# Performance work log

Measured on AMD Instinct MI355X. Metric: run time of the kernel, lower is better.

The kernel has to match this reference:

```python
import jax, jax.numpy as jnp
import numpy as np

D = 2048  # input_size
H = 2048  # hidden_size
K = 4096  # number of children


def setup_inputs() -> dict:
    key = jax.random.key(0)
    ks = jax.random.split(key, 12)
    sD = 1.0 / np.sqrt(D)
    sH = 1.0 / np.sqrt(H)
    return {
        "input": jax.random.normal(ks[0], (D,), dtype=jnp.float32),
        "children_c": jax.random.normal(ks[1], (K, H), dtype=jnp.float32),
        "children_h": jax.random.normal(ks[2], (K, H), dtype=jnp.float32),
        "W_iou_x": jax.random.uniform(ks[3], (3 * H, D), jnp.float32, -sD, sD),
        "b_iou_x": jax.random.uniform(ks[4], (3 * H,), jnp.float32, -sD, sD),
        "W_iou_h": jax.random.uniform(ks[5], (3 * H, H), jnp.float32, -sH, sH),
        "b_iou_h": jax.random.uniform(ks[6], (3 * H,), jnp.float32, -sH, sH),
        "W_fx": jax.random.uniform(ks[7], (H, D), jnp.float32, -sD, sD),
        "b_fx": jax.random.uniform(ks[8], (H,), jnp.float32, -sD, sD),
        "W_fh": jax.random.uniform(ks[9], (H, H), jnp.float32, -sH, sH),
        "b_fh": jax.random.uniform(ks[10], (H,), jnp.float32, -sH, sH),
    }


def reference(input, children_c, children_h,
              W_iou_x, b_iou_x, W_iou_h, b_iou_h,
              W_fx, b_fx, W_fh, b_fh):
    # iou = iou_x(input) + iou_h(sum_k h_k)  -> [3H]
    h_sum = jnp.sum(children_h, axis=0)
    iou = (W_iou_x @ input + b_iou_x) + (W_iou_h @ h_sum + b_iou_h)
    i, o, u = jnp.split(iou, 3)
    i = jax.nn.sigmoid(i)
    o = jax.nn.sigmoid(o)
    u = jnp.tanh(u)
    # per-child forget gates, batched over K (original loops in Python):
    # f_k = sigmoid(f_x(input) + f_h(h_k))  -> [K, H]
    fx = W_fx @ input + b_fx                       # [H], computed once
    fh = children_h @ W_fh.T + b_fh                # [K, H] GEMM
    f = jax.nn.sigmoid(fx[None, :] + fh)           # [K, H]
    c = i * u + jnp.sum(f * children_c, axis=0)    # [H]
    h = o * jnp.tanh(c)                            # [H]
    return (o, c, h)
```

## Files before the change

### kernel.cpp

```cpp
#include <hip/hip_runtime.h>

typedef unsigned short u16;
typedef short bf16x8 __attribute__((ext_vector_type(8)));
typedef float f32x4 __attribute__((ext_vector_type(4)));

#define D_IN 2048
#define H_DIM 2048
#define K_CH 4096

__device__ __forceinline__ u16 f2bf(float f) {
  unsigned int u = __float_as_uint(f);
  u += 0x7fffu + ((u >> 16) & 1u);
  return (u16)(u >> 16);
}
__device__ __forceinline__ float sigmoidf(float x) {
  return 1.0f / (1.0f + __expf(-x));
}
__device__ __forceinline__ uint4 packrow(float4 a, float4 b) {
  uint4 w;
  w.x = (unsigned)f2bf(a.x) | ((unsigned)f2bf(a.y) << 16);
  w.y = (unsigned)f2bf(a.z) | ((unsigned)f2bf(a.w) << 16);
  w.z = (unsigned)f2bf(b.x) | ((unsigned)f2bf(b.y) << 16);
  w.w = (unsigned)f2bf(b.z) | ((unsigned)f2bf(b.w) << 16);
  return w;
}

__global__ __launch_bounds__(256) void k1(
    const float* __restrict__ ch, const float* __restrict__ wfh,
    const float* __restrict__ Wfx, const float* __restrict__ bfx,
    const float* __restrict__ bfh, const float* __restrict__ x,
    const float* __restrict__ Wix, const float* __restrict__ bix,
    const float* __restrict__ bih, float* __restrict__ partials,
    u16* __restrict__ chb, u16* __restrict__ wfhb, float* __restrict__ g,
    float* __restrict__ ioux, float* __restrict__ hsum,
    float* __restrict__ accv) {
  const int t = threadIdx.x;
  const int bid = blockIdx.x;
  if (bid < 1024) {
    const int r0 = bid * 4;
    float4 a[4], b[4];
#pragma unroll
    for (int r = 0; r < 4; ++r) {
      const float4* p = (const float4*)(ch + (size_t)(r0 + r) * H_DIM + t * 8);
      a[r] = p[0];
      b[r] = p[1];
    }
    float s0 = 0.f, s1 = 0.f, s2 = 0.f, s3 = 0.f;
    float s4 = 0.f, s5 = 0.f, s6 = 0.f, s7 = 0.f;
#pragma unroll
    for (int r = 0; r < 4; ++r) {
      s0 += a[r].x; s1 += a[r].y; s2 += a[r].z; s3 += a[r].w;
      s4 += b[r].x; s5 += b[r].y; s6 += b[r].z; s7 += b[r].w;
      *(uint4*)(chb + (size_t)(r0 + r) * H_DIM + t * 8) = packrow(a[r], b[r]);
    }
    float4 lo, hi;
    lo.x = s0; lo.y = s1; lo.z = s2; lo.w = s3;
    hi.x = s4; hi.y = s5; hi.z = s6; hi.w = s7;
    float* pp = partials + (size_t)bid * H_DIM + t * 8;
    *(float4*)pp = lo;
    *(float4*)(pp + 4) = hi;
  } else if (bid < 1536) {
    const size_t base = (size_t)(bid - 1024) * 8192 + t * 8;
    float4 a[4], b[4];
#pragma unroll
    for (int j = 0; j < 4; ++j) {
      const float4* p = (const float4*)(wfh + base + j * 2048);
      a[j] = p[0];
      b[j] = p[1];
    }
#pragma unroll
    for (int j = 0; j < 4; ++j)
      *(uint4*)(wfhb + base + j * 2048) = packrow(a[j], b[j]);
  } else if (bid < 2048) {
    const int wave = t >> 6, lane = t & 63;
    const int h = (bid - 1536) * 4 + wave;
    const float4* w = (const float4*)(Wfx + (size_t)h * D_IN);
    const float4* xv = (const float4*)x;
    float s = 0.f;
#pragma unroll
    for (int i = 0; i < 8; ++i) {
      int idx = i * 64 + lane;
      float4 av = w[idx], bv = xv[idx];
      s += av.x * bv.x + av.y * bv.y + av.z * bv.z + av.w * bv.w;
    }
#pragma unroll
    for (int off = 32; off > 0; off >>= 1) s += __shfl_xor(s, off);
    if (lane == 0) g[h] = s + bfx[h] + bfh[h];
  } else if (bid < 3584) {
    const int wave = t >> 6, lane = t & 63;
    const int row = (bid - 2048) * 4 + wave;
    const float4* w = (const float4*)(Wix + (size_t)row * D_IN);
    const float4* xv = (const float4*)x;
    float s = 0.f;
#pragma unroll
    for (int i = 0; i < 8; ++i) {
      int idx = i * 64 + lane;
      float4 av = w[idx], bv = xv[idx];
      s += av.x * bv.x + av.y * bv.y + av.z * bv.z + av.w * bv.w;
    }
#pragma unroll
    for (int off = 32; off > 0; off >>= 1) s += __shfl_xor(s, off);
    if (lane == 0) ioux[row] = s + bix[row] + bih[row];
  } else {
    float4 z = {0.f, 0.f, 0.f, 0.f};
    ((float4*)hsum)[t * 2] = z;
    ((float4*)hsum)[t * 2 + 1] = z;
    ((float4*)accv)[t * 2] = z;
    ((float4*)accv)[t * 2 + 1] = z;
  }
}

#define BM 256
#define BN 128
#define BK 64

__global__ __launch_bounds__(512) void kG(
    const u16* __restrict__ chb, const float* __restrict__ cc,
    const u16* __restrict__ wfhb, const float* __restrict__ g,
    const float* __restrict__ partials, float* __restrict__ hsum,
    float* __restrict__ accv) {
  __shared__ u16 As[2][BM * BK];
  __shared__ u16 Bs[2][BN * BK];

  const int bid = blockIdx.x;
  const int t = threadIdx.x;

  if (bid < 64) {
    const int c = (bid & 7) * 256 + (t & 255);
    const int p0 = (bid >> 3) * 128 + (t >> 8) * 64;
    float a0 = 0.f, a1 = 0.f, a2 = 0.f, a3 = 0.f;
    float a4 = 0.f, a5 = 0.f, a6 = 0.f, a7 = 0.f;
    for (int p = p0; p < p0 + 64; p += 8) {
      a0 += partials[(size_t)(p + 0) * H_DIM + c];
      a1 += partials[(size_t)(p + 1) * H_DIM + c];
      a2 += partials[(size_t)(p + 2) * H_DIM + c];
      a3 += partials[(size_t)(p + 3) * H_DIM + c];
      a4 += partials[(size_t)(p + 4) * H_DIM + c];
      a5 += partials[(size_t)(p + 5) * H_DIM + c];
      a6 += partials[(size_t)(p + 6) * H_DIM + c];
      a7 += partials[(size_t)(p + 7) * H_DIM + c];
    }
    float s = ((a0 + a1) + (a2 + a3)) + ((a4 + a5) + (a6 + a7));
    atomicAdd(hsum + c, s);
    return;
  }

  const int gb = bid - 64;
  const int xcd = gb & 7;
  const int u = gb >> 3;
  const int bm = (xcd << 1) | (u >> 4);
  const int bn = u & 15;
  const int row0 = bm * BM;
  const int col0 = bn * BN;

  const int wave = t >> 6, lane = t & 63;
  const int lrow = lane & 15, lquad = lane >> 4;
  const int wm = wave >> 1, wn = wave & 1;

  f32x4 acc[4][4] = {};

  const int srow = lane >> 3;
  const int schunk = (lane & 7) ^ srow;
  const u16* agbase = chb  + (size_t)(row0 + wave * 32 + srow) * H_DIM + schunk * 8;
  const u16* bgbase = wfhb + (size_t)(col0 + wave * 16 + srow) * H_DIM + schunk * 8;

#define STAGE(buf, kb)                                                        \
  do {                                                                        \
    _Pragma("unroll")                                                         \
    for (int i = 0; i < 4; ++i)                                               \
      __builtin_amdgcn_global_load_lds(                                       \
          (const __attribute__((address_space(1))) void*)(agbase + (size_t)i * 8 * H_DIM + (kb) * BK), \
          (__attribute__((address_space(3))) void*)(&As[buf][(wave * 32 + i * 8) * 64]), \
          16, 0, 0);                                                          \
    _Pragma("unroll")                                                         \
    for (int i = 0; i < 2; ++i)                                               \
      __builtin_amdgcn_global_load_lds(                                       \
          (const __attribute__((address_space(1))) void*)(bgbase + (size_t)i * 8 * H_DIM + (kb) * BK), \
          (__attribute__((address_space(3))) void*)(&Bs[buf][(wave * 16 + i * 8) * 64]), \
          16, 0, 0);                                                          \
  } while (0)

#define COMPUTE(buf)                                                          \
  do {                                                                        \
    _Pragma("unroll")                                                         \
    for (int step = 0; step < 2; ++step) {                                    \
      const int slot = ((step * 4 + lquad) ^ (lrow & 7)) * 8;                 \
      bf16x8 fa[4], fb[4];                                                    \
      _Pragma("unroll")                                                       \
      for (int i = 0; i < 4; ++i)                                             \
        fa[i] = *(const bf16x8*)(&As[buf][(wm * 64 + i * 16 + lrow) * 64 + slot]); \
      _Pragma("unroll")                                                       \
      for (int i = 0; i < 4; ++i)                                             \
        fb[i] = *(const bf16x8*)(&Bs[buf][(wn * 64 + i * 16 + lrow) * 64 + slot]); \
      __builtin_amdgcn_s_setprio(1);                                          \
      _Pragma("unroll")                                                       \
      for (int mi = 0; mi < 4; ++mi)                                          \
        _Pragma("unroll")                                                     \
        for (int ni = 0; ni < 4; ++ni)                                        \
          acc[mi][ni] = __builtin_amdgcn_mfma_f32_16x16x32_bf16(              \
              fa[mi], fb[ni], acc[mi][ni], 0, 0, 0);                          \
      __builtin_amdgcn_s_setprio(0);                                          \
    }                                                                         \
  } while (0)

#define VMCNT6() do { asm volatile("s_waitcnt vmcnt(6)" ::: "memory");        \
                      __builtin_amdgcn_sched_barrier(0); } while (0)
#define VMCNT0() do { asm volatile("s_waitcnt vmcnt(0)" ::: "memory");        \
                      __builtin_amdgcn_sched_barrier(0); } while (0)
#define SBAR()   do { __builtin_amdgcn_s_barrier();                           \
                      __builtin_amdgcn_sched_barrier(0); } while (0)

  STAGE(0, 0);
  STAGE(1, 1);

  for (int kb = 0; kb < D_IN / BK - 2; ++kb) {
    const int cur = kb & 1;
    VMCNT6();
    SBAR();
    COMPUTE(cur);
    SBAR();
    STAGE(cur, kb + 2);
  }
  VMCNT6(); SBAR();
  COMPUTE(0);
  SBAR();
  VMCNT0(); SBAR();
  COMPUTE(1);

#pragma unroll
  for (int ni = 0; ni < 4; ++ni) {
    const int colg = col0 + wn * 64 + ni * 16 + lrow;
    const float gv = g[colg];
    float s = 0.f;
#pragma unroll
    for (int mi = 0; mi < 4; ++mi) {
      const int rowg = row0 + wm * 64 + mi * 16 + lquad * 4;
#pragma unroll
      for (int r = 0; r < 4; ++r) {
        float f = sigmoidf(gv + acc[mi][ni][r]);
        s += f * cc[(size_t)(rowg + r) * H_DIM + colg];
      }
    }
    s += __shfl_xor(s, 16);
    s += __shfl_xor(s, 32);
    if (lquad == 0) atomicAdd(accv + colg, s);
  }
#undef STAGE
#undef COMPUTE
#undef VMCNT6
#undef VMCNT0
#undef SBAR
}

__global__ __launch_bounds__(256) void kmvF(const float* __restrict__ Wih,
                                            const float* __restrict__ hsum,
                                            const float* __restrict__ ioux,
                                            const float* __restrict__ accv,
                                            float* __restrict__ out) {
  const int wave = threadIdx.x >> 6, lane = threadIdx.x & 63;
  const int h = blockIdx.x * 4 + wave;
  const float4* w0 = (const float4*)(Wih + (size_t)h * H_DIM);
  const float4* w1 = (const float4*)(Wih + (size_t)(H_DIM + h) * H_DIM);
  const float4* w2 = (const float4*)(Wih + (size_t)(2 * H_DIM + h) * H_DIM);
  const float4* hv = (const float4*)hsum;
  float s0 = 0.f, s1 = 0.f, s2 = 0.f;
#pragma unroll
  for (int i = 0; i < 8; ++i) {
    int idx = i * 64 + lane;
    float4 b = hv[idx];
    float4 a0 = w0[idx], a1 = w1[idx], a2 = w2[idx];
    s0 += a0.x * b.x + a0.y * b.y + a0.z * b.z + a0.w * b.w;
    s1 += a1.x * b.x + a1.y * b.y + a1.z * b.z + a1.w * b.w;
    s2 += a2.x * b.x + a2.y * b.y + a2.z * b.z + a2.w * b.w;
  }
#pragma unroll
  for (int off = 32; off > 0; off >>= 1) {
    s0 += __shfl_xor(s0, off);
    s1 += __shfl_xor(s1, off);
    s2 += __shfl_xor(s2, off);
  }
  if (lane == 0) {
    float i_ = sigmoidf(ioux[h] + s0);
    float o_ = sigmoidf(ioux[H_DIM + h] + s1);
    float u_ = tanhf(ioux[2 * H_DIM + h] + s2);
    float c_ = i_ * u_ + accv[h];
    float hh = o_ * tanhf(c_);
    out[h] = o_;
    out[H_DIM + h] = c_;
    out[2 * H_DIM + h] = hh;
  }
}

extern "C" void kernel_launch(void* const* d_in, const int* in_sizes, int n_in,
                              void* d_out, int out_size, void* d_ws, size_t ws_size,
                              hipStream_t stream) {
  const float* x   = (const float*)d_in[0];
  const float* cc  = (const float*)d_in[1];
  const float* ch  = (const float*)d_in[2];
  const float* Wix = (const float*)d_in[3];
  const float* bix = (const float*)d_in[4];
  const float* Wih = (const float*)d_in[5];
  const float* bih = (const float*)d_in[6];
  const float* Wfx = (const float*)d_in[7];
  const float* bfx = (const float*)d_in[8];
  const float* Wfh = (const float*)d_in[9];
  const float* bfh = (const float*)d_in[10];

  float* ws   = (float*)d_ws;
  float* hsum = ws;
  float* ioux = ws + 2048;
  float* g    = ws + 8192;
  float* accv = ws + 10240;
  float* partials = ws + 12288;
  u16* chb  = (u16*)(ws + 12288 + 1024 * 2048);
  u16* wfhb = chb + (size_t)K_CH * H_DIM;
  float* out = (float*)d_out;

  k1<<<3585, 256, 0, stream>>>(ch, Wfh, Wfx, bfx, bfh, x, Wix, bix, bih,
                               partials, chb, wfhb, g, ioux, hsum, accv);
  kG<<<320, 512, 0, stream>>>(chb, cc, wfhb, g, partials, hsum, accv);
  kmvF<<<512, 256, 0, stream>>>(Wih, hsum, ioux, accv, out);
}
```

Baseline: 258.8 us.

## Triple-buffer LDS and double-buffer register fragments in forget-gate GEMM

Moves the GEMM main loop from two LDS buffers to three with rotating indices. It also double-buffers the MFMA operand fragments in registers, so the LDS reads for the next tile are issued while the MFMAs for the current tile run. The goal is to hide LDS read latency and global-load latency behind matrix-core work. The cost is more LDS per block (lower occupancy possible), double the fragment registers, and more delicate waitcnt accounting that could be wrong.

```diff
diff --git a/kernel.cpp b/kernel.cpp
--- a/kernel.cpp
+++ b/kernel.cpp
@@ -119,8 +119,8 @@
     const u16* __restrict__ wfhb, const float* __restrict__ g,
     const float* __restrict__ partials, float* __restrict__ hsum,
     float* __restrict__ accv) {
-  __shared__ u16 As[2][BM * BK];
-  __shared__ u16 Bs[2][BN * BK];
+  __shared__ u16 As[3][BM * BK];
+  __shared__ u16 Bs[3][BN * BK];
 
   const int bid = blockIdx.x;
   const int t = threadIdx.x;
@@ -158,74 +158,100 @@
   const int wm = wave >> 1, wn = wave & 1;
 
   f32x4 acc[4][4] = {};
+  bf16x8 faA[2][4], fbA[2][4];
+  bf16x8 faB[2][4], fbB[2][4];
 
   const int srow = lane >> 3;
   const int schunk = (lane & 7) ^ srow;
   const u16* agbase = chb  + (size_t)(row0 + wave * 32 + srow) * H_DIM + schunk * 8;
   const u16* bgbase = wfhb + (size_t)(col0 + wave * 16 + srow) * H_DIM + schunk * 8;
 
-#define STAGE(buf, kb)                                                        \
+#define STAGE(bi, kb)                                                         \
   do {                                                                        \
     _Pragma("unroll")                                                         \
     for (int i = 0; i < 4; ++i)                                               \
       __builtin_amdgcn_global_load_lds(                                       \
-          (const __attribute__((address_space(1))) void*)(agbase + (size_t)i * 8 * H_DIM + (kb) * BK), \
-          (__attribute__((address_space(3))) void*)(&As[buf][(wave * 32 + i * 8) * 64]), \
+          (const __attribute__((address_space(1))) void*)(agbase + (size_t)i * 8 * H_DIM + (size_t)(kb) * BK), \
+          (__attribute__((address_space(3))) void*)(&As[bi][(wave * 32 + i * 8) * 64]), \
           16, 0, 0);                                                          \
     _Pragma("unroll")                                                         \
     for (int i = 0; i < 2; ++i)                                               \
       __builtin_amdgcn_global_load_lds(                                       \
-          (const __attribute__((address_space(1))) void*)(bgbase + (size_t)i * 8 * H_DIM + (kb) * BK), \
-          (__attribute__((address_space(3))) void*)(&Bs[buf][(wave * 16 + i * 8) * 64]), \
+          (const __attribute__((address_space(1))) void*)(bgbase + (size_t)i * 8 * H_DIM + (size_t)(kb) * BK), \
+          (__attribute__((address_space(3))) void*)(&Bs[bi][(wave * 16 + i * 8) * 64]), \
           16, 0, 0);                                                          \
   } while (0)
 
-#define COMPUTE(buf)                                                          \
+#define READ_SET(fax, fbx, bi)                                                \
   do {                                                                        \
     _Pragma("unroll")                                                         \
     for (int step = 0; step < 2; ++step) {                                    \
       const int slot = ((step * 4 + lquad) ^ (lrow & 7)) * 8;                 \
-      bf16x8 fa[4], fb[4];                                                    \
       _Pragma("unroll")                                                       \
       for (int i = 0; i < 4; ++i)                                             \
-        fa[i] = *(const bf16x8*)(&As[buf][(wm * 64 + i * 16 + lrow) * 64 + slot]); \
+        fax[step][i] = *(const bf16x8*)(&As[bi][(wm * 64 + i * 16 + lrow) * 64 + slot]); \
       _Pragma("unroll")                                                       \
       for (int i = 0; i < 4; ++i)                                             \
-        fb[i] = *(const bf16x8*)(&Bs[buf][(wn * 64 + i * 16 + lrow) * 64 + slot]); \
-      __builtin_amdgcn_s_setprio(1);                                          \
+        fbx[step][i] = *(const bf16x8*)(&Bs[bi][(wn * 64 + i * 16 + lrow) * 64 + slot]); \
+    }                                                                         \
+  } while (0)
+
+#define COMPUTE_SET(fax, fbx)                                                 \
+  do {                                                                        \
+    __builtin_amdgcn_s_setprio(1);                                            \
+    _Pragma("unroll")                                                         \
+    for (int step = 0; step < 2; ++step)                                      \
       _Pragma("unroll")                                                       \
       for (int mi = 0; mi < 4; ++mi)                                          \
         _Pragma("unroll")                                                     \
         for (int ni = 0; ni < 4; ++ni)                                        \
           acc[mi][ni] = __builtin_amdgcn_mfma_f32_16x16x32_bf16(              \
-              fa[mi], fb[ni], acc[mi][ni], 0, 0, 0);                          \
-      __builtin_amdgcn_s_setprio(0);                                          \
-    }                                                                         \
+              fax[step][mi], fbx[step][ni], acc[mi][ni], 0, 0, 0);            \
+    __builtin_amdgcn_s_setprio(0);                                            \
   } while (0)
 
 #define VMCNT6() do { asm volatile("s_waitcnt vmcnt(6)" ::: "memory");        \
                       __builtin_amdgcn_sched_barrier(0); } while (0)
 #define VMCNT0() do { asm volatile("s_waitcnt vmcnt(0)" ::: "memory");        \
+                      __builtin_amdgcn_sched_barrier(0); } while (0)
+#define LGKM15() do { asm volatile("s_waitcnt lgkmcnt(15)" ::: "memory");     \
+                      __builtin_amdgcn_sched_barrier(0); } while (0)
+#define LGKM0()  do { asm volatile("s_waitcnt lgkmcnt(0)" ::: "memory");      \
                       __builtin_amdgcn_sched_barrier(0); } while (0)
 #define SBAR()   do { __builtin_amdgcn_s_barrier();                           \
                       __builtin_amdgcn_sched_barrier(0); } while (0)
 
   STAGE(0, 0);
   STAGE(1, 1);
-
-  for (int kb = 0; kb < D_IN / BK - 2; ++kb) {
-    const int cur = kb & 1;
+  VMCNT6();
+  SBAR();
+  READ_SET(faA, fbA, 0);
+
+  int c0 = 0, c1 = 1, c2 = 2;
+  for (int kb = 0; kb < 30; kb += 2) {
+    STAGE(c2, kb + 2);
     VMCNT6();
     SBAR();
-    COMPUTE(cur);
+    READ_SET(faB, fbB, c1);
+    LGKM15();
+    COMPUTE_SET(faA, fbA);
     SBAR();
-    STAGE(cur, kb + 2);
-  }
-  VMCNT6(); SBAR();
-  COMPUTE(0);
+    STAGE(c0, kb + 3);
+    VMCNT6();
+    SBAR();
+    READ_SET(faA, fbA, c2);
+    LGKM15();
+    COMPUTE_SET(faB, fbB);
+    SBAR();
+    const int tmp = c0; c0 = c2; c2 = c1; c1 = tmp;
+  }
+  VMCNT0();
   SBAR();
-  VMCNT0(); SBAR();
-  COMPUTE(1);
+  READ_SET(faB, fbB, 1);
+  LGKM15();
+  COMPUTE_SET(faA, fbA);
+  LGKM0();
+  COMPUTE_SET(faB, fbB);
 
 #pragma unroll
   for (int ni = 0; ni < 4; ++ni) {
@@ -246,9 +272,12 @@
     if (lquad == 0) atomicAdd(accv + colg, s);
   }
 #undef STAGE
-#undef COMPUTE
+#undef READ_SET
+#undef COMPUTE_SET
 #undef VMCNT6
 #undef VMCNT0
+#undef LGKM15
+#undef LGKM0
 #undef SBAR
 }
 
```

Measured after the change: 256.0 us. About the same (-1.1%).
